# Performance work log

Measured on AMD Instinct MI355X. Metric: run time of the kernel, lower is better.

The kernel has to match this reference:

```python
import jax, jax.numpy as jnp
import numpy as np


def _block_causal_mask(cu_seqlens, seq_len):
    """Boolean [seq_len, seq_len] mask: True = attend (same doc AND causal)."""
    positions = jnp.arange(seq_len)
    # searchsorted(side='right') - 1 maps each position to its document id
    seq_ids = jnp.searchsorted(cu_seqlens, positions, side='right') - 1
    same_seq = seq_ids[:, None] == seq_ids[None, :]
    causal = positions[None, :] <= positions[:, None]
    return same_seq & causal


def setup_inputs() -> dict:
    key = jax.random.key(0)
    kq, kk, kv, kc = jax.random.split(key, 4)
    B, H, S, D = 1, 16, 4096, 128
    q = jax.random.normal(kq, (B, H, S, D), dtype=jnp.float32)
    k = jax.random.normal(kk, (B, H, S, D), dtype=jnp.float32)
    v = jax.random.normal(kv, (B, H, S, D), dtype=jnp.float32)
    # 8 packed documents: interior boundaries are sorted random ints in (0, S)
    inner = jnp.sort(jax.random.randint(kc, (7,), 1, S, dtype=jnp.int64))
    cu_seqlens = jnp.concatenate([
        jnp.zeros((1,), jnp.int64), inner, jnp.full((1,), S, jnp.int64)
    ])
    return {"q": q, "k": k, "v": v, "cu_seqlens": cu_seqlens, "max_seqlen": S}


def reference(q, k, v, cu_seqlens, max_seqlen):
    # q, k, v: [B, H, S, D]; block-diagonal causal SDPA over packed sequences.
    S, D = q.shape[2], q.shape[3]
    scale = 1.0 / jnp.sqrt(jnp.asarray(D, q.dtype))
    allow = _block_causal_mask(cu_seqlens, S)  # [S, S] bool
    scores = jnp.einsum('bhsd,bhtd->bhst', q, k) * scale  # [B, H, S, S]
    neg_inf = jnp.asarray(-jnp.inf, scores.dtype)
    scores = jnp.where(allow[None, None], scores, neg_inf)
    probs = jax.nn.softmax(scores, axis=-1)
    return jnp.einsum('bhst,bhtd->bhsd', probs, v)
```

## Files before the change

### kernel.cpp

```cpp
#include <hip/hip_runtime.h>

typedef float  f32x4  __attribute__((ext_vector_type(4)));
typedef __bf16 bf16x8 __attribute__((ext_vector_type(8)));
typedef unsigned short u16;
typedef u16 u16x8 __attribute__((ext_vector_type(8)));
typedef u16 u16x4 __attribute__((ext_vector_type(4)));

#define HEADS 16
#define DIM   128
#define QT    64
#define KTILE 64
#define PSTR  72
#define KSTR  136
#define VSTR  68

__device__ __forceinline__ u16 f2bf(float f) {
    unsigned u = __builtin_bit_cast(unsigned, f);
    u += 0x7FFFu + ((u >> 16) & 1u);
    return (u16)(u >> 16);
}

__device__ __forceinline__ void dma16(const void* g, void* l) {
    auto* gp = (const __attribute__((address_space(1))) unsigned*)(uintptr_t)g;
    auto* lp = (__attribute__((address_space(3))) unsigned*)(uintptr_t)l;
    __builtin_amdgcn_global_load_lds(gp, lp, 16, 0, 0);
}

__global__ __launch_bounds__(256) void prep_kv(
    const float* __restrict__ K, const float* __restrict__ V,
    u16* __restrict__ KB, u16* __restrict__ VB, int S)
{
    __shared__ __align__(16) u16 T[128 * 72];
    int nt = S >> 6;
    int tile = blockIdx.x % nt, h = blockIdx.x / nt;
    int t = threadIdx.x;
    long tb = (long)(h * nt + tile) * 8192;

    const float* ksrc = K + ((long)(h * S + tile * 64)) * DIM;
#pragma unroll
    for (int it = 0; it < 4; ++it) {
        int idx = t + it * 256;
        int g = idx & 15, r = idx >> 4;
        const float* src = ksrc + (long)r * DIM + g * 8;
        f32x4 a = *(const f32x4*)src;
        f32x4 b = *(const f32x4*)(src + 4);
        u16x8 o;
        o[0]=f2bf(a[0]); o[1]=f2bf(a[1]); o[2]=f2bf(a[2]); o[3]=f2bf(a[3]);
        o[4]=f2bf(b[0]); o[5]=f2bf(b[1]); o[6]=f2bf(b[2]); o[7]=f2bf(b[3]);
        *(u16x8*)&KB[tb + r * 128 + ((g ^ (r & 7)) << 3)] = o;
    }

    int col4 = (t & 31) * 4;
    int row  = t >> 5;
    const float* vsrc = V + ((long)(h * S + tile * 64)) * DIM;
#pragma unroll
    for (int it = 0; it < 8; ++it) {
        int k = row + it * 8;
        f32x4 x = *(const f32x4*)(vsrc + (long)k * DIM + col4);
        T[(col4 + 0) * 72 + k] = f2bf(x[0]);
        T[(col4 + 1) * 72 + k] = f2bf(x[1]);
        T[(col4 + 2) * 72 + k] = f2bf(x[2]);
        T[(col4 + 3) * 72 + k] = f2bf(x[3]);
    }
    __syncthreads();
#pragma unroll
    for (int it = 0; it < 4; ++it) {
        int idx = t + it * 256;
        int d = idx >> 3, g2 = idx & 7;
        u16x8 o = *(const u16x8*)&T[d * 72 + g2 * 8];
        *(u16x8*)&VB[tb + d * 64 + ((g2 ^ (d & 7)) << 3)] = o;
    }
}

__global__ __launch_bounds__(256, 2) void fa_main(
    const float* __restrict__ Q, const u16* __restrict__ KB,
    const u16* __restrict__ VB, const void* __restrict__ cu_raw,
    int n_cu, float* __restrict__ O, int S, int n_qb)
{
    __shared__ __align__(16) u16 Kb[2][64 * 128];
    __shared__ __align__(16) u16 Vt[2][128 * 64];
    __shared__ __align__(16) u16 On[16 * 64];
    __shared__ __align__(16) u16 Pw[4][16 * PSTR];
    __shared__ int cu_s[32];

    const int tid  = threadIdx.x;
    const int wave = tid >> 6, lane = tid & 63;
    const int quad = lane >> 4, l16 = lane & 15;
    const int h  = blockIdx.x & (HEADS - 1);
    const int qb = (n_qb - 1) - (blockIdx.x >> 4);
    const int q0 = qb * QT;

    {
        const int* cu32 = (const int*)cu_raw;
        bool is64 = (cu32[1] == 0);
        for (int t = tid; t < n_cu; t += blockDim.x)
            cu_s[t] = is64 ? (int)((const long long*)cu_raw)[t] : cu32[t];
    }
    for (int i = tid; i < 1024; i += 256)
        On[i] = (i < 64) ? (u16)0x3F80 : (u16)0;
    __syncthreads();

    const float sc2 = 0.08838834764831845f * 1.4426950408889634f;
    const long hb = (long)h * S * DIM;
    const long hk = (long)h * (S >> 6) * 8192;
    const int qend = q0 + QT;

    int qstart[4];
#pragma unroll
    for (int r = 0; r < 4; ++r) {
        int qi = q0 + wave * 16 + quad * 4 + r;
        int st = 0;
        for (int j = 0; j < n_cu; ++j) if (cu_s[j] <= qi) st = cu_s[j];
        qstart[r] = st;
    }
    int q0s = 0;
    for (int j = 0; j < n_cu; ++j) if (cu_s[j] <= q0) q0s = cu_s[j];

    bf16x8 qfrag[4];
    {
        const float* qp = Q + hb + (long)(q0 + wave * 16 + l16) * DIM + quad * 8;
#pragma unroll
        for (int kk = 0; kk < 4; ++kk) {
            f32x4 x = *(const f32x4*)(qp + kk * 32);
            f32x4 y = *(const f32x4*)(qp + kk * 32 + 4);
            u16x8 u;
            u[0]=f2bf(x[0]); u[1]=f2bf(x[1]); u[2]=f2bf(x[2]); u[3]=f2bf(x[3]);
            u[4]=f2bf(y[0]); u[5]=f2bf(y[1]); u[6]=f2bf(y[2]); u[7]=f2bf(y[3]);
            qfrag[kk] = __builtin_bit_cast(bf16x8, u);
        }
    }

    f32x4 acc[9];
#pragma unroll
    for (int dt = 0; dt < 9; ++dt) acc[dt] = (f32x4){0.f, 0.f, 0.f, 0.f};

    const int t0 = (q0s & ~(KTILE - 1)) >> 6;
    const int ntile = (qend >> 6) - t0;
    const u16* ksrc = KB + hk;
    const u16* vsrc = VB + hk;

    {
        long off = (long)t0 * 8192;
#pragma unroll
        for (int c = 0; c < 4; ++c) {
            int ch = wave * 4 + c;
            dma16(ksrc + off + ch * 512 + lane * 8, &Kb[0][ch * 512]);
            dma16(vsrc + off + ch * 512 + lane * 8, &Vt[0][ch * 512]);
        }
    }

    for (int i = 0; i < ntile; ++i) {
        const int cur = i & 1;
        if (i + 1 < ntile) {
            long off = (long)(t0 + i + 1) * 8192;
#pragma unroll
            for (int c = 0; c < 4; ++c) {
                int ch = wave * 4 + c;
                dma16(ksrc + off + ch * 512 + lane * 8, &Kb[cur ^ 1][ch * 512]);
                dma16(vsrc + off + ch * 512 + lane * 8, &Vt[cur ^ 1][ch * 512]);
            }
            asm volatile("s_waitcnt vmcnt(8)" ::: "memory");
        } else {
            asm volatile("s_waitcnt vmcnt(0)" ::: "memory");
        }
        __builtin_amdgcn_s_barrier();

        const int kt = (t0 + i) << 6;
        const u16* kb = &Kb[cur][0];
        const u16* vt = &Vt[cur][0];

        f32x4 sc[4];
#pragma unroll
        for (int nt = 0; nt < 4; ++nt) sc[nt] = (f32x4){0.f, 0.f, 0.f, 0.f};
        __builtin_amdgcn_s_setprio(1);
#pragma unroll
        for (int kk = 0; kk < 4; ++kk)
#pragma unroll
            for (int nt = 0; nt < 4; ++nt) {
                int row = nt * 16 + l16;
                int g = kk * 4 + quad;
                u16x8 bu = *(const u16x8*)&kb[row * 128 + ((g ^ (row & 7)) << 3)];
                sc[nt] = __builtin_amdgcn_mfma_f32_16x16x32_bf16(
                    qfrag[kk], __builtin_bit_cast(bf16x8, bu), sc[nt], 0, 0, 0);
            }
        __builtin_amdgcn_s_setprio(0);

#pragma unroll
        for (int nt = 0; nt < 4; ++nt) {
            int kj = kt + nt * 16 + l16;
#pragma unroll
            for (int r = 0; r < 4; ++r) {
                int qi = q0 + wave * 16 + quad * 4 + r;
                bool ok = (kj >= qstart[r]) && (kj <= qi);
                float pv = ok ? __builtin_amdgcn_exp2f(sc[nt][r] * sc2) : 0.f;
                Pw[wave][(quad*4 + r) * PSTR + ((nt ^ quad) * 16 + l16)] = f2bf(pv);
            }
        }

        __builtin_amdgcn_s_setprio(1);
#pragma unroll
        for (int kk2 = 0; kk2 < 2; ++kk2) {
            int colx = (kk2*32 + quad*8) ^ ((l16 >> 2) << 4);
            u16x8 au = *(const u16x8*)&Pw[wave][l16 * PSTR + colx];
            bf16x8 ap = __builtin_bit_cast(bf16x8, au);
            int g2 = kk2 * 4 + quad;
#pragma unroll
            for (int dt = 0; dt < 8; ++dt) {
                int d = dt * 16 + l16;
                u16x8 bu = *(const u16x8*)&vt[(d << 6) + ((g2 ^ (d & 7)) << 3)];
                acc[dt] = __builtin_amdgcn_mfma_f32_16x16x32_bf16(
                    ap, __builtin_bit_cast(bf16x8, bu), acc[dt], 0, 0, 0);
            }
            {
                u16x8 bo = *(const u16x8*)&On[(l16 << 6) + ((g2 ^ (l16 & 7)) << 3)];
                acc[8] = __builtin_amdgcn_mfma_f32_16x16x32_bf16(
                    ap, __builtin_bit_cast(bf16x8, bo), acc[8], 0, 0, 0);
            }
        }
        __builtin_amdgcn_s_setprio(0);

        __builtin_amdgcn_s_barrier();
    }

#pragma unroll
    for (int r = 0; r < 4; ++r) {
        float l = __shfl(acc[8][r], (lane & 48), 64);
        int qi = q0 + wave * 16 + quad * 4 + r;
        float inv = 1.f / l;
        float* op = O + hb + (long)qi * DIM + l16;
#pragma unroll
        for (int dt = 0; dt < 8; ++dt)
            op[dt * 16] = acc[dt][r] * inv;
    }
}

__global__ __launch_bounds__(256, 2) void fa_fallback(
    const float* __restrict__ Q, const float* __restrict__ K,
    const float* __restrict__ V, const void* __restrict__ cu_raw,
    int n_cu, float* __restrict__ O, int S)
{
    __shared__ __align__(16) u16 Kb[KTILE * KSTR];
    __shared__ __align__(16) u16 Vt[DIM * VSTR];
    __shared__ __align__(16) u16 Pw[4][16 * PSTR];
    __shared__ int cu_s[32];

    const int tid  = threadIdx.x;
    const int wave = tid >> 6, lane = tid & 63;
    const int quad = lane >> 4, l16 = lane & 15;
    const int q0   = blockIdx.x * QT;
    const int h    = blockIdx.y;
    const int cg = tid & 31, rr = tid >> 5;
    const int dv = tid & 127, hiv = tid >> 7;

    {
        const int* cu32 = (const int*)cu_raw;
        bool is64 = (cu32[1] == 0);
        for (int t = tid; t < n_cu; t += blockDim.x)
            cu_s[t] = is64 ? (int)((const long long*)cu_raw)[t] : cu32[t];
    }
    __syncthreads();

    const long hb = (long)h * S * DIM;
    const float NEG_INF = -__builtin_inff();
    const float scale = 0.08838834764831845f;

    int qstart[4];
#pragma unroll
    for (int r = 0; r < 4; ++r) {
        int qi = q0 + wave * 16 + quad * 4 + r;
        int st = 0;
        for (int j = 0; j < n_cu; ++j) if (cu_s[j] <= qi) st = cu_s[j];
        qstart[r] = st;
    }
    int q0s = 0;
    for (int j = 0; j < n_cu; ++j) if (cu_s[j] <= q0) q0s = cu_s[j];

    bf16x8 qfrag[4];
    {
        const float* qp = Q + hb + (long)(q0 + wave * 16 + l16) * DIM + quad * 8;
#pragma unroll
        for (int kk = 0; kk < 4; ++kk) {
            f32x4 x = *(const f32x4*)(qp + kk * 32);
            f32x4 y = *(const f32x4*)(qp + kk * 32 + 4);
            u16x8 u;
            u[0]=f2bf(x[0]); u[1]=f2bf(x[1]); u[2]=f2bf(x[2]); u[3]=f2bf(x[3]);
            u[4]=f2bf(y[0]); u[5]=f2bf(y[1]); u[6]=f2bf(y[2]); u[7]=f2bf(y[3]);
            qfrag[kk] = __builtin_bit_cast(bf16x8, u);
        }
    }

    f32x4 acc[8];
#pragma unroll
    for (int dt = 0; dt < 8; ++dt) acc[dt] = (f32x4){0.f, 0.f, 0.f, 0.f};
    float m_r[4], l_r[4];
#pragma unroll
    for (int r = 0; r < 4; ++r) { m_r[r] = NEG_INF; l_r[r] = 0.f; }

    for (int kt = q0s & ~(KTILE - 1); kt < q0 + QT; kt += KTILE) {
        __syncthreads();
        {
#pragma unroll
            for (int it = 0; it < 8; ++it) {
                f32x4 kx = *(const f32x4*)(K + hb + (long)(kt + rr + it*8) * DIM + cg*4);
                u16x4 kb4;
                kb4[0]=f2bf(kx[0]); kb4[1]=f2bf(kx[1]);
                kb4[2]=f2bf(kx[2]); kb4[3]=f2bf(kx[3]);
                *(u16x4*)&Kb[(rr + it*8) * KSTR + cg*4] = kb4;
            }
#pragma unroll
            for (int p = 0; p < 8; ++p) {
                int kq = 2*p + hiv;
                const float* vp = V + hb + (long)(kt + kq*4) * DIM + dv;
                u16x4 w;
                w[0]=f2bf(vp[0]); w[1]=f2bf(vp[(long)DIM]);
                w[2]=f2bf(vp[(long)2*DIM]); w[3]=f2bf(vp[(long)3*DIM]);
                *(u16x4*)&Vt[dv * VSTR + kq*4] = w;
            }
        }
        __syncthreads();

        f32x4 sc[4];
#pragma unroll
        for (int nt = 0; nt < 4; ++nt) sc[nt] = (f32x4){0.f, 0.f, 0.f, 0.f};
#pragma unroll
        for (int kk = 0; kk < 4; ++kk)
#pragma unroll
            for (int nt = 0; nt < 4; ++nt) {
                u16x8 bu = *(const u16x8*)&Kb[(nt*16 + l16) * KSTR + kk*32 + quad*8];
                sc[nt] = __builtin_amdgcn_mfma_f32_16x16x32_bf16(
                    qfrag[kk], __builtin_bit_cast(bf16x8, bu), sc[nt], 0, 0, 0);
            }
#pragma unroll
        for (int nt = 0; nt < 4; ++nt) {
            int kj = kt + nt * 16 + l16;
#pragma unroll
            for (int r = 0; r < 4; ++r) {
                int qi = q0 + wave * 16 + quad * 4 + r;
                bool ok = (kj >= qstart[r]) && (kj <= qi);
                sc[nt][r] = ok ? sc[nt][r] * scale : NEG_INF;
            }
        }
        float mnew[4], alpha[4], rsum[4];
#pragma unroll
        for (int r = 0; r < 4; ++r) {
            float tm = fmaxf(fmaxf(sc[0][r], sc[1][r]), fmaxf(sc[2][r], sc[3][r]));
#pragma unroll
            for (int off = 1; off < 16; off <<= 1)
                tm = fmaxf(tm, __shfl_xor(tm, off, 64));
            float mn = fmaxf(m_r[r], tm);
            mnew[r]  = mn;
            alpha[r] = (mn == NEG_INF) ? 1.f : __expf(m_r[r] - mn);
            rsum[r]  = 0.f;
        }
#pragma unroll
        for (int nt = 0; nt < 4; ++nt)
#pragma unroll
            for (int r = 0; r < 4; ++r) {
                float pv = (sc[nt][r] == NEG_INF) ? 0.f : __expf(sc[nt][r] - mnew[r]);
                sc[nt][r] = pv;
                rsum[r] += pv;
            }
#pragma unroll
        for (int r = 0; r < 4; ++r) {
            float s = rsum[r];
#pragma unroll
            for (int off = 1; off < 16; off <<= 1) s += __shfl_xor(s, off, 64);
            l_r[r] = l_r[r] * alpha[r] + s;
            m_r[r] = mnew[r];
        }
#pragma unroll
        for (int dt = 0; dt < 8; ++dt)
#pragma unroll
            for (int r = 0; r < 4; ++r) acc[dt][r] *= alpha[r];

#pragma unroll
        for (int nt = 0; nt < 4; ++nt)
#pragma unroll
            for (int r = 0; r < 4; ++r)
                Pw[wave][(quad*4 + r) * PSTR + ((nt ^ quad) * 16 + l16)] = f2bf(sc[nt][r]);

#pragma unroll
        for (int kk2 = 0; kk2 < 2; ++kk2) {
            int colx = (kk2*32 + quad*8) ^ ((l16 >> 2) << 4);
            u16x8 au = *(const u16x8*)&Pw[wave][l16 * PSTR + colx];
            bf16x8 ap = __builtin_bit_cast(bf16x8, au);
#pragma unroll
            for (int dt = 0; dt < 8; ++dt) {
                int base = (dt*16 + l16) * VSTR + kk2*32 + quad*8;
                u16x4 lo = *(const u16x4*)&Vt[base];
                u16x4 hi = *(const u16x4*)&Vt[base + 4];
                u16x8 bu;
                bu[0]=lo[0]; bu[1]=lo[1]; bu[2]=lo[2]; bu[3]=lo[3];
                bu[4]=hi[0]; bu[5]=hi[1]; bu[6]=hi[2]; bu[7]=hi[3];
                acc[dt] = __builtin_amdgcn_mfma_f32_16x16x32_bf16(
                    ap, __builtin_bit_cast(bf16x8, bu), acc[dt], 0, 0, 0);
            }
        }
    }

#pragma unroll
    for (int r = 0; r < 4; ++r) {
        int qi = q0 + wave * 16 + quad * 4 + r;
        float inv = 1.f / l_r[r];
        float* op = O + hb + (long)qi * DIM + l16;
#pragma unroll
        for (int dt = 0; dt < 8; ++dt)
            op[dt * 16] = acc[dt][r] * inv;
    }
}

extern "C" void kernel_launch(void* const* d_in, const int* in_sizes, int n_in,
                              void* d_out, int out_size, void* d_ws, size_t ws_size,
                              hipStream_t stream) {
    const float* q = (const float*)d_in[0];
    const float* k = (const float*)d_in[1];
    const float* v = (const float*)d_in[2];
    const void* cu = d_in[3];
    int n_cu = in_sizes[3];
    int S = in_sizes[0] / (HEADS * DIM);
    size_t perMat = (size_t)HEADS * S * 256;
    if (ws_size >= 2 * perMat) {
        u16* KB = (u16*)d_ws;
        u16* VB = (u16*)((char*)d_ws + perMat);
        prep_kv<<<dim3(HEADS * (S >> 6)), 256, 0, stream>>>(k, v, KB, VB, S);
        int n_qb = S / QT;
        fa_main<<<dim3(n_qb * HEADS), 256, 0, stream>>>(
            q, KB, VB, cu, n_cu, (float*)d_out, S, n_qb);
    } else {
        fa_fallback<<<dim3(S / QT, HEADS), 256, 0, stream>>>(
            q, k, v, cu, n_cu, (float*)d_out, S);
    }
}
```

Baseline: 186.6 us.

## Keep softmax probabilities in registers via transposed QK MFMA and permlane swaps

Swaps the MFMA operands for QK^T so each lane holds scores for its own query row. The probabilities are packed to bf16 with v_cvt_pk_bf16_f32 and rearranged into the PV A-operand layout with permlane32/permlane16 swaps, which removes the per-wave LDS staging buffer Pw and its store/load round trip. The mask is now computed per lane with a single document-start lookup. The main risk is a wrong lane permutation mapping, which would give incorrect results.

```diff
diff --git a/kernel.cpp b/kernel.cpp
--- a/kernel.cpp
+++ b/kernel.cpp
@@ -5,6 +5,7 @@
 typedef unsigned short u16;
 typedef u16 u16x8 __attribute__((ext_vector_type(8)));
 typedef u16 u16x4 __attribute__((ext_vector_type(4)));
+typedef unsigned u32x4 __attribute__((ext_vector_type(4)));
 
 #define HEADS 16
 #define DIM   128
@@ -24,6 +25,12 @@
     auto* gp = (const __attribute__((address_space(1))) unsigned*)(uintptr_t)g;
     auto* lp = (__attribute__((address_space(3))) unsigned*)(uintptr_t)l;
     __builtin_amdgcn_global_load_lds(gp, lp, 16, 0, 0);
+}
+
+__device__ __forceinline__ unsigned cvtpk(float lo, float hi) {
+    unsigned r;
+    asm("v_cvt_pk_bf16_f32 %0, %1, %2" : "=v"(r) : "v"(lo), "v"(hi));
+    return r;
 }
 
 __global__ __launch_bounds__(256) void prep_kv(
@@ -80,7 +87,6 @@
     __shared__ __align__(16) u16 Kb[2][64 * 128];
     __shared__ __align__(16) u16 Vt[2][128 * 64];
     __shared__ __align__(16) u16 On[16 * 64];
-    __shared__ __align__(16) u16 Pw[4][16 * PSTR];
     __shared__ int cu_s[32];
 
     const int tid  = threadIdx.x;
@@ -105,14 +111,9 @@
     const long hk = (long)h * (S >> 6) * 8192;
     const int qend = q0 + QT;
 
-    int qstart[4];
-#pragma unroll
-    for (int r = 0; r < 4; ++r) {
-        int qi = q0 + wave * 16 + quad * 4 + r;
-        int st = 0;
-        for (int j = 0; j < n_cu; ++j) if (cu_s[j] <= qi) st = cu_s[j];
-        qstart[r] = st;
-    }
+    const int qi_l = q0 + wave * 16 + l16;
+    int qs = 0;
+    for (int j = 0; j < n_cu; ++j) if (cu_s[j] <= qi_l) qs = cu_s[j];
     int q0s = 0;
     for (int j = 0; j < n_cu; ++j) if (cu_s[j] <= q0) q0s = cu_s[j];
 
@@ -181,28 +182,40 @@
                 int g = kk * 4 + quad;
                 u16x8 bu = *(const u16x8*)&kb[row * 128 + ((g ^ (row & 7)) << 3)];
                 sc[nt] = __builtin_amdgcn_mfma_f32_16x16x32_bf16(
-                    qfrag[kk], __builtin_bit_cast(bf16x8, bu), sc[nt], 0, 0, 0);
+                    __builtin_bit_cast(bf16x8, bu), qfrag[kk], sc[nt], 0, 0, 0);
             }
         __builtin_amdgcn_s_setprio(0);
 
+        float p[4][4];
 #pragma unroll
         for (int nt = 0; nt < 4; ++nt) {
-            int kj = kt + nt * 16 + l16;
 #pragma unroll
             for (int r = 0; r < 4; ++r) {
-                int qi = q0 + wave * 16 + quad * 4 + r;
-                bool ok = (kj >= qstart[r]) && (kj <= qi);
-                float pv = ok ? __builtin_amdgcn_exp2f(sc[nt][r] * sc2) : 0.f;
-                Pw[wave][(quad*4 + r) * PSTR + ((nt ^ quad) * 16 + l16)] = f2bf(pv);
-            }
+                int kj = kt + nt * 16 + quad * 4 + r;
+                bool ok = (kj >= qs) && (kj <= qi_l);
+                p[nt][r] = ok ? __builtin_amdgcn_exp2f(sc[nt][r] * sc2) : 0.f;
+            }
+        }
+
+        unsigned Ra[4], Rb[4];
+#pragma unroll
+        for (int nt = 0; nt < 4; ++nt) {
+            Ra[nt] = cvtpk(p[nt][0], p[nt][1]);
+            Rb[nt] = cvtpk(p[nt][2], p[nt][3]);
         }
 
         __builtin_amdgcn_s_setprio(1);
 #pragma unroll
         for (int kk2 = 0; kk2 < 2; ++kk2) {
-            int colx = (kk2*32 + quad*8) ^ ((l16 >> 2) << 4);
-            u16x8 au = *(const u16x8*)&Pw[wave][l16 * PSTR + colx];
-            bf16x8 ap = __builtin_bit_cast(bf16x8, au);
+            unsigned a0 = Ra[2*kk2], a1 = Ra[2*kk2 + 1];
+            unsigned b0 = Rb[2*kk2], b1 = Rb[2*kk2 + 1];
+            asm("v_permlane32_swap_b32 %0, %1" : "+v"(a0), "+v"(a1));
+            asm("v_permlane16_swap_b32 %0, %1" : "+v"(a0), "+v"(a1));
+            asm("v_permlane32_swap_b32 %0, %1" : "+v"(b0), "+v"(b1));
+            asm("v_permlane16_swap_b32 %0, %1" : "+v"(b0), "+v"(b1));
+            u32x4 wv; wv[0] = a0; wv[1] = b0; wv[2] = a1; wv[3] = b1;
+            bf16x8 ap = __builtin_bit_cast(bf16x8, wv);
+
             int g2 = kk2 * 4 + quad;
 #pragma unroll
             for (int dt = 0; dt < 8; ++dt) {
```

Result: faster. 174.8 us (-6.3%).
